# Kernel tuning notes

Measured on AMD Instinct MI355X. Metric: run time of the kernel, lower is better.

Reference implementation:

```python
import jax, jax.numpy as jnp
import numpy as np
import math

N = 50000        # nodes
E = 800000       # edges
FEATS = 64
CLASSES = 16
HIDDEN = 64
DEPTH = 10
DIFF = 0.9
EMB_DIM = 1 + int(math.log2(FEATS))   # 7
ADJ_HID = 4 + EMB_DIM                  # 11


def setup_inputs() -> dict:
    key = jax.random.key(0)
    ks = jax.random.split(key, 12)
    x = jax.random.normal(ks[0], (N, FEATS), dtype=jnp.float32)
    src = jax.random.randint(ks[1], (E,), 0, N, dtype=jnp.int64)
    dst = jax.random.randint(ks[2], (E,), 0, N, dtype=jnp.int64)
    s = 0.05
    W1 = jax.random.normal(ks[3], (2 * FEATS, HIDDEN), jnp.float32) * s
    b1 = jnp.zeros((HIDDEN,), jnp.float32)
    W2 = jax.random.normal(ks[4], (HIDDEN, CLASSES), jnp.float32) * s
    b2 = jnp.zeros((CLASSES,), jnp.float32)
    A1 = jax.random.normal(ks[5], (2 + EMB_DIM, ADJ_HID), jnp.float32) * s
    ab1 = jnp.zeros((ADJ_HID,), jnp.float32)
    A2 = jax.random.normal(ks[6], (ADJ_HID, 1), jnp.float32) * s
    ab2 = jnp.zeros((1,), jnp.float32)
    emb = jax.random.normal(ks[7], (FEATS, EMB_DIM), jnp.float32) * s
    return {"x": x, "src": src, "dst": dst, "W1": W1, "b1": b1,
            "W2": W2, "b2": b2, "A1": A1, "ab1": ab1, "A2": A2,
            "ab2": ab2, "emb": emb}


def reference(x, src, dst, W1, b1, W2, b2, A1, ab1, A2, ab2, emb):
    n, f = x.shape
    # cached symmetric GCN normalization: D^-1/2 A D^-1/2
    deg = jax.ops.segment_sum(jnp.ones((src.shape[0],), x.dtype), dst, num_segments=n)
    inv_sqrt = jnp.where(deg > 0, jax.lax.rsqrt(jnp.maximum(deg, 1e-12)), 0.0)
    norm = inv_sqrt[src] * inv_sqrt[dst]   # [E]

    def conv(z):
        return jax.ops.segment_sum(z[src] * norm[:, None], dst, num_segments=n)

    # first diffusion loop (personalized-pagerank style residual blend)
    h0 = x
    z = x
    for _ in range(DEPTH):
        z = conv(z) * DIFF + (1.0 - DIFF) * h0

    # node x class pair MLP (class-major flatten, matching x.t().reshape(-1,1))
    cls = jnp.repeat(jnp.arange(f), n)                 # [f*n]
    pairs = jnp.concatenate([z.T.reshape(-1, 1),
                             h0.T.reshape(-1, 1),
                             emb[cls]], axis=1)        # [f*n, 2+EMB_DIM]
    u = jax.nn.relu(pairs @ A1 + ab1)
    u = (u @ A2 + ab2) / 2.0                           # [f*n, 1]
    z = u.reshape(f, n).T                              # [n, f]

    # dropout is identity in eval mode
    z = jnp.concatenate([z, h0], axis=1)               # [n, 2f]
    z = jax.nn.relu(z @ W1 + b1)
    z = z @ W2 + b2                                    # [n, classes]

    # second diffusion loop over class logits
    g0 = z
    for _ in range(DEPTH):
        z = conv(z) * DIFF + (1.0 - DIFF) * g0
    return z
```

## Files before the change

kernel.cpp:

```cpp
#include <hip/hip_runtime.h>

#define FEATS    64
#define CLASSES  16
#define EMB_DIM  7
#define ADJ_HID  11
#define DIFF     0.9f

__device__ inline float bf2f(unsigned short u) {
    return __uint_as_float(((unsigned int)u) << 16);
}
__device__ inline unsigned short f2bf(float f) {
    unsigned int u = __float_as_uint(f);
    return (unsigned short)((u + 0x7FFFu + ((u >> 16) & 1u)) >> 16);
}


__global__ __launch_bounds__(256) void k_deg(const int* __restrict__ dst, int* __restrict__ deg, int e) {
    int i = blockIdx.x * 256 + threadIdx.x;
    if (i < e) atomicAdd(&deg[dst[i]], 1);
}

__global__ __launch_bounds__(256) void k_invs(const int* __restrict__ deg, float* __restrict__ invs, int n) {
    int i = blockIdx.x * 256 + threadIdx.x;
    if (i < n) { int d = deg[i]; invs[i] = d > 0 ? rsqrtf((float)d) : 0.f; }
}

__global__ __launch_bounds__(256) void k_scan1(const int* __restrict__ deg, int* __restrict__ rowptr,
                                               int* __restrict__ bsum, int n) {
    __shared__ int s[256];
    int tid = threadIdx.x;
    int i = blockIdx.x * 256 + tid;
    int v = (i < n) ? deg[i] : 0;
    s[tid] = v; __syncthreads();
    for (int ofs = 1; ofs < 256; ofs <<= 1) {
        int t = (tid >= ofs) ? s[tid - ofs] : 0;
        __syncthreads(); s[tid] += t; __syncthreads();
    }
    if (i < n) rowptr[i] = s[tid] - v;
    if (tid == 255) bsum[blockIdx.x] = s[255];
}

__global__ __launch_bounds__(256) void k_scan2(int* __restrict__ bsum, int nb) {
    __shared__ int s[256];
    int tid = threadIdx.x;
    int v = (tid < nb) ? bsum[tid] : 0;
    s[tid] = v; __syncthreads();
    for (int ofs = 1; ofs < 256; ofs <<= 1) {
        int t = (tid >= ofs) ? s[tid - ofs] : 0;
        __syncthreads(); s[tid] += t; __syncthreads();
    }
    if (tid < nb) bsum[tid] = s[tid] - v;
}

__global__ __launch_bounds__(256) void k_scan3(int* __restrict__ rowptr, const int* __restrict__ bsum,
                                               int n, int e) {
    int i = blockIdx.x * 256 + threadIdx.x;
    if (i < n) rowptr[i] += bsum[i >> 8];
    if (i == n) rowptr[n] = e;
}

__global__ __launch_bounds__(256) void k_scatter(const int* __restrict__ src, const int* __restrict__ dst,
                                                 const float* __restrict__ invs, const int* __restrict__ rowptr,
                                                 int* __restrict__ cnt, int2* __restrict__ edge, int e) {
    int i = blockIdx.x * 256 + threadIdx.x;
    if (i >= e) return;
    int d = dst[i], sv = src[i];
    int pos = rowptr[d] + atomicAdd(&cnt[d], 1);
    edge[pos] = make_int2(sv, __float_as_int(invs[sv] * invs[d]));
}


__global__ __launch_bounds__(256) void k_cast(const float4* __restrict__ in, ushort4* __restrict__ out, int total4) {
    int i = blockIdx.x * 256 + threadIdx.x;
    if (i < total4) {
        float4 v = in[i];
        ushort4 o;
        o.x = f2bf(v.x); o.y = f2bf(v.y); o.z = f2bf(v.z); o.w = f2bf(v.w);
        out[i] = o;
    }
}


__global__ __launch_bounds__(256) void k_conv64b(const ushort4* __restrict__ zin, const float4* __restrict__ h04,
                                                 ushort4* __restrict__ zout, const int* __restrict__ rowptr,
                                                 const int2* __restrict__ edge, int n) {
    int wid = (blockIdx.x * 256 + threadIdx.x) >> 6;
    if (wid >= n) return;
    int lane = threadIdx.x & 63;
    int g = lane >> 4, c = lane & 15;
    int e0 = rowptr[wid], e1 = rowptr[wid + 1];
    float a0 = 0.f, a1 = 0.f, a2 = 0.f, a3 = 0.f;
    for (int e = e0; e < e1; e += 16) {
        #pragma unroll
        for (int k = 0; k < 4; ++k) {
            int idx = e + k * 4 + g;
            bool ok = idx < e1;
            int2 p = edge[ok ? idx : e0];
            float w = ok ? __int_as_float(p.y) : 0.f;
            ushort4 v = zin[(size_t)p.x * 16 + c];
            a0 = fmaf(w, bf2f(v.x), a0);
            a1 = fmaf(w, bf2f(v.y), a1);
            a2 = fmaf(w, bf2f(v.z), a2);
            a3 = fmaf(w, bf2f(v.w), a3);
        }
    }
    a0 += __shfl_xor(a0, 16); a1 += __shfl_xor(a1, 16);
    a2 += __shfl_xor(a2, 16); a3 += __shfl_xor(a3, 16);
    a0 += __shfl_xor(a0, 32); a1 += __shfl_xor(a1, 32);
    a2 += __shfl_xor(a2, 32); a3 += __shfl_xor(a3, 32);
    if (lane < 16) {
        float4 h = h04[(size_t)wid * 16 + lane];
        ushort4 o;
        o.x = f2bf(a0 * DIFF + (1.f - DIFF) * h.x);
        o.y = f2bf(a1 * DIFF + (1.f - DIFF) * h.y);
        o.z = f2bf(a2 * DIFF + (1.f - DIFF) * h.z);
        o.w = f2bf(a3 * DIFF + (1.f - DIFF) * h.w);
        zout[(size_t)wid * 16 + lane] = o;
    }
}


__global__ __launch_bounds__(256) void k_conv16(const float4* __restrict__ zin4, const float4* __restrict__ g04,
                                                float4* __restrict__ zout4, const int* __restrict__ rowptr,
                                                const int2* __restrict__ edge, int n) {
    int wid = (blockIdx.x * 256 + threadIdx.x) >> 6;
    if (wid >= n) return;
    int lane = threadIdx.x & 63;
    int g = lane >> 2, c = lane & 3;
    int e0 = rowptr[wid], e1 = rowptr[wid + 1];
    float4 acc; acc.x = acc.y = acc.z = acc.w = 0.f;
    for (int e = e0; e < e1; e += 32) {
        #pragma unroll
        for (int k = 0; k < 2; ++k) {
            int idx = e + k * 16 + g;
            bool ok = idx < e1;
            int2 p = edge[ok ? idx : e0];
            float w = ok ? __int_as_float(p.y) : 0.f;
            float4 v = zin4[(size_t)p.x * 4 + c];
            acc.x = fmaf(w, v.x, acc.x);
            acc.y = fmaf(w, v.y, acc.y);
            acc.z = fmaf(w, v.z, acc.z);
            acc.w = fmaf(w, v.w, acc.w);
        }
    }
    float4 t;
    t.x = __shfl_xor(acc.x, 4);  t.y = __shfl_xor(acc.y, 4);  t.z = __shfl_xor(acc.z, 4);  t.w = __shfl_xor(acc.w, 4);
    acc.x += t.x; acc.y += t.y; acc.z += t.z; acc.w += t.w;
    t.x = __shfl_xor(acc.x, 8);  t.y = __shfl_xor(acc.y, 8);  t.z = __shfl_xor(acc.z, 8);  t.w = __shfl_xor(acc.w, 8);
    acc.x += t.x; acc.y += t.y; acc.z += t.z; acc.w += t.w;
    t.x = __shfl_xor(acc.x, 16); t.y = __shfl_xor(acc.y, 16); t.z = __shfl_xor(acc.z, 16); t.w = __shfl_xor(acc.w, 16);
    acc.x += t.x; acc.y += t.y; acc.z += t.z; acc.w += t.w;
    t.x = __shfl_xor(acc.x, 32); t.y = __shfl_xor(acc.y, 32); t.z = __shfl_xor(acc.z, 32); t.w = __shfl_xor(acc.w, 32);
    acc.x += t.x; acc.y += t.y; acc.z += t.z; acc.w += t.w;
    if (lane < 4) {
        float4 h = g04[(size_t)wid * 4 + lane];
        float4 o;
        o.x = acc.x * DIFF + (1.f - DIFF) * h.x;
        o.y = acc.y * DIFF + (1.f - DIFF) * h.y;
        o.z = acc.z * DIFF + (1.f - DIFF) * h.z;
        o.w = acc.w * DIFF + (1.f - DIFF) * h.w;
        zout4[(size_t)wid * 4 + lane] = o;
    }
}


__global__ __launch_bounds__(256) void k_pairmlp(const unsigned short* __restrict__ z1, const float* __restrict__ x,
                                                 const float* __restrict__ W1, const float* __restrict__ b1,
                                                 const float* __restrict__ W2, const float* __restrict__ b2,
                                                 const float* __restrict__ A1, const float* __restrict__ ab1,
                                                 const float* __restrict__ A2, const float* __restrict__ ab2,
                                                 const float* __restrict__ emb,
                                                 float* __restrict__ g0, int n) {
    __shared__ float W2s[64 * 16];
    __shared__ float in_s[32][128];
    __shared__ float hid[32 * 65];
    __shared__ float eA1[64 * ADJ_HID];
    __shared__ float a0s[ADJ_HID], a1s[ADJ_HID], a2s[ADJ_HID];
    __shared__ float ab2s;

    int tid  = threadIdx.x;
    int base = blockIdx.x * 32;

    #pragma unroll
    for (int k = 0; k < 4; ++k)  W2s[tid + k * 256] = W2[tid + k * 256];
    if (tid < ADJ_HID) { a0s[tid] = A1[tid]; a1s[tid] = A1[ADJ_HID + tid]; a2s[tid] = A2[tid]; }
    if (tid == 0) ab2s = ab2[0];
    for (int idx = tid; idx < 64 * ADJ_HID; idx += 256) {
        int c = idx / ADJ_HID, h = idx - c * ADJ_HID;
        float s = ab1[h];
        #pragma unroll
        for (int j = 0; j < EMB_DIM; j++) s = fmaf(emb[c * EMB_DIM + j], A1[(2 + j) * ADJ_HID + h], s);
        eA1[idx] = s;
    }
    __syncthreads();

    #pragma unroll
    for (int k = 0; k < 8; ++k) {
        int idx = tid + k * 256;
        int nl = idx >> 6, c = idx & 63;
        int node = base + nl; if (node > n - 1) node = n - 1;
        float zv = bf2f(z1[(size_t)node * 64 + c]);
        float xv = x[(size_t)node * 64 + c];
        float out = ab2s;
        #pragma unroll
        for (int h = 0; h < ADJ_HID; h++) {
            float t = fmaf(zv, a0s[h], fmaf(xv, a1s[h], eA1[c * ADJ_HID + h]));
            t = fmaxf(t, 0.f);
            out = fmaf(t, a2s[h], out);
        }
        in_s[nl][c]      = out * 0.5f;
        in_s[nl][64 + c] = xv;
    }
    __syncthreads();

    {
        int lane = tid & 63, wv = tid >> 6;
        int nb0 = wv * 8;
        float bv = b1[lane];
        float acc[8];
        #pragma unroll
        for (int j = 0; j < 8; ++j) acc[j] = bv;
        #pragma unroll 8
        for (int rb = 0; rb < 128; rb += 4) {
            float w0 = W1[(rb    ) * 64 + lane];
            float w1 = W1[(rb + 1) * 64 + lane];
            float w2 = W1[(rb + 2) * 64 + lane];
            float w3 = W1[(rb + 3) * 64 + lane];
            #pragma unroll
            for (int j = 0; j < 8; ++j) {
                float4 iv = *(const float4*)&in_s[nb0 + j][rb];
                acc[j] = fmaf(iv.w, w3, fmaf(iv.z, w2, fmaf(iv.y, w1, fmaf(iv.x, w0, acc[j]))));
            }
        }
        #pragma unroll
        for (int j = 0; j < 8; ++j) hid[(nb0 + j) * 65 + lane] = fmaxf(acc[j], 0.f);
    }
    __syncthreads();

    {
        int c  = tid & 15;
        int nl = tid >> 4;
        float ac0 = b2[c], ac1 = ac0;
        #pragma unroll
        for (int h = 0; h < 64; ++h) {
            float w = W2s[h * 16 + c];
            ac0 = fmaf(hid[nl * 65 + h],        w, ac0);
            ac1 = fmaf(hid[(nl + 16) * 65 + h], w, ac1);
        }
        int n0 = base + nl, n1 = base + nl + 16;
        if (n0 < n) g0[(size_t)n0 * 16 + c] = ac0;
        if (n1 < n) g0[(size_t)n1 * 16 + c] = ac1;
    }
}


extern "C" void kernel_launch(void* const* d_in, const int* in_sizes, int n_in,
                              void* d_out, int out_size, void* d_ws, size_t ws_size,
                              hipStream_t stream) {
    const float* x   = (const float*)d_in[0];
    const int*   src = (const int*)d_in[1];
    const int*   dst = (const int*)d_in[2];
    const float* W1  = (const float*)d_in[3];
    const float* b1  = (const float*)d_in[4];
    const float* W2  = (const float*)d_in[5];
    const float* b2  = (const float*)d_in[6];
    const float* A1  = (const float*)d_in[7];
    const float* ab1 = (const float*)d_in[8];
    const float* A2  = (const float*)d_in[9];
    const float* ab2 = (const float*)d_in[10];
    const float* emb = (const float*)d_in[11];

    int n = in_sizes[0] / FEATS;
    int e = in_sizes[1];

    char* ws = (char*)d_ws;
    size_t off = 0;
    auto alloc = [&](size_t bytes) {
        void* p = ws + off;
        off += bytes;
        off = (off + 255) & ~(size_t)255;
        return p;
    };

    int*     deg    = (int*)    alloc((size_t)n * 4);
    float*   invs   = (float*)  alloc((size_t)n * 4);
    int*     rowptr = (int*)    alloc((size_t)(n + 1) * 4);
    int*     cnt    = (int*)    alloc((size_t)n * 4);
    int*     bsum   = (int*)    alloc(1024);
    int2*    edge   = (int2*)   alloc((size_t)e * 8 + 256);
    ushort4* zbA    = (ushort4*)alloc((size_t)n * 64 * 2);
    ushort4* zbB    = (ushort4*)alloc((size_t)n * 64 * 2);
    float*   g0     = (float*)  alloc((size_t)n * 16 * 4);
    float*   g1     = (float*)  alloc((size_t)n * 16 * 4);
    float*   g2     = (float*)  alloc((size_t)n * 16 * 4);

    hipMemsetAsync(deg, 0, (size_t)n * 4, stream);
    hipMemsetAsync(cnt, 0, (size_t)n * 4, stream);

    int eb = (e + 255) / 256;
    int nb = (n + 255) / 256;

    k_deg    <<<eb, 256, 0, stream>>>(dst, deg, e);
    k_invs   <<<nb, 256, 0, stream>>>(deg, invs, n);
    k_scan1  <<<nb, 256, 0, stream>>>(deg, rowptr, bsum, n);
    k_scan2  <<<1, 256, 0, stream>>>(bsum, nb);
    k_scan3  <<<(n + 256) / 256, 256, 0, stream>>>(rowptr, bsum, n, e);
    k_scatter<<<eb, 256, 0, stream>>>(src, dst, invs, rowptr, cnt, edge, e);

    int total4 = n * 16;
    k_cast<<<(total4 + 255) / 256, 256, 0, stream>>>((const float4*)x, zbA, total4);

    int nwb = (n + 3) / 4;

    const ushort4* zin = zbA;
    ushort4* zout = zbB;
    for (int it = 0; it < 10; ++it) {
        k_conv64b<<<nwb, 256, 0, stream>>>(zin, (const float4*)x, zout, rowptr, edge, n);
        zin  = zout;
        zout = (zout == zbA) ? zbB : zbA;
    }
    const unsigned short* z1 = (const unsigned short*)zin;

    k_pairmlp<<<(n + 31) / 32, 256, 0, stream>>>(z1, x, W1, b1, W2, b2,
                                                 A1, ab1, A2, ab2, emb, g0, n);

    const float* gin = g0;
    float* gout = g1;
    for (int it = 0; it < 10; ++it) {
        float* out = (it == 9) ? (float*)d_out : gout;
        k_conv16<<<nwb, 256, 0, stream>>>((const float4*)gin, (const float4*)g0, (float4*)out,
                                          rowptr, edge, n);
        gin  = out;
        gout = (gout == g1) ? g2 : g1;
    }
}
```

Measured before the change: 706.1 us.

## Use bf16 residual in diffusion and persistent pair-MLP with shared-memory W1

The first diffusion loop now reads its residual h0 from a bf16 copy of x instead of fp32, which halves that read traffic in every iteration. The pair-MLP kernel becomes persistent with a fixed grid of 512 blocks looping over tiles. It stages W1 in shared memory once per block and vectorises the pair computation with ushort4/float4 loads and a transposed eA1 table. The bf16 residual adds rounding error to h0, and the kernel now uses about 50KB of shared memory, which can limit occupancy.

```diff
diff --git a/kernel.cpp b/kernel.cpp
--- a/kernel.cpp
+++ b/kernel.cpp
@@ -81,7 +81,7 @@
 }
 
 
-__global__ __launch_bounds__(256) void k_conv64b(const ushort4* __restrict__ zin, const float4* __restrict__ h04,
+__global__ __launch_bounds__(256) void k_conv64b(const ushort4* __restrict__ zin, const ushort4* __restrict__ h0b,
                                                  ushort4* __restrict__ zout, const int* __restrict__ rowptr,
                                                  const int2* __restrict__ edge, int n) {
     int wid = (blockIdx.x * 256 + threadIdx.x) >> 6;
@@ -109,12 +109,12 @@
     a0 += __shfl_xor(a0, 32); a1 += __shfl_xor(a1, 32);
     a2 += __shfl_xor(a2, 32); a3 += __shfl_xor(a3, 32);
     if (lane < 16) {
-        float4 h = h04[(size_t)wid * 16 + lane];
+        ushort4 h4 = h0b[(size_t)wid * 16 + lane];
         ushort4 o;
-        o.x = f2bf(a0 * DIFF + (1.f - DIFF) * h.x);
-        o.y = f2bf(a1 * DIFF + (1.f - DIFF) * h.y);
-        o.z = f2bf(a2 * DIFF + (1.f - DIFF) * h.z);
-        o.w = f2bf(a3 * DIFF + (1.f - DIFF) * h.w);
+        o.x = f2bf(a0 * DIFF + (1.f - DIFF) * bf2f(h4.x));
+        o.y = f2bf(a1 * DIFF + (1.f - DIFF) * bf2f(h4.y));
+        o.z = f2bf(a2 * DIFF + (1.f - DIFF) * bf2f(h4.z));
+        o.w = f2bf(a3 * DIFF + (1.f - DIFF) * bf2f(h4.w));
         zout[(size_t)wid * 16 + lane] = o;
     }
 }
@@ -164,92 +164,108 @@
 }
 
 
+#define PM_GRID 512
+
 __global__ __launch_bounds__(256) void k_pairmlp(const unsigned short* __restrict__ z1, const float* __restrict__ x,
                                                  const float* __restrict__ W1, const float* __restrict__ b1,
                                                  const float* __restrict__ W2, const float* __restrict__ b2,
                                                  const float* __restrict__ A1, const float* __restrict__ ab1,
                                                  const float* __restrict__ A2, const float* __restrict__ ab2,
                                                  const float* __restrict__ emb,
-                                                 float* __restrict__ g0, int n) {
+                                                 float* __restrict__ g0, int n, int ntiles) {
+    __shared__ float W1s[128 * 64];
     __shared__ float W2s[64 * 16];
     __shared__ float in_s[32][128];
     __shared__ float hid[32 * 65];
-    __shared__ float eA1[64 * ADJ_HID];
+    __shared__ float eA1T[ADJ_HID * 64];
     __shared__ float a0s[ADJ_HID], a1s[ADJ_HID], a2s[ADJ_HID];
     __shared__ float ab2s;
 
-    int tid  = threadIdx.x;
-    int base = blockIdx.x * 32;
-
+    int tid = threadIdx.x;
+    const ushort4* z4p = (const ushort4*)z1;
+    const float4*  x4p = (const float4*)x;
+
+    #pragma unroll
+    for (int k = 0; k < 32; ++k) W1s[tid + k * 256] = W1[tid + k * 256];
     #pragma unroll
     for (int k = 0; k < 4; ++k)  W2s[tid + k * 256] = W2[tid + k * 256];
     if (tid < ADJ_HID) { a0s[tid] = A1[tid]; a1s[tid] = A1[ADJ_HID + tid]; a2s[tid] = A2[tid]; }
     if (tid == 0) ab2s = ab2[0];
-    for (int idx = tid; idx < 64 * ADJ_HID; idx += 256) {
-        int c = idx / ADJ_HID, h = idx - c * ADJ_HID;
+    for (int idx = tid; idx < ADJ_HID * 64; idx += 256) {
+        int h = idx >> 6, c = idx & 63;
         float s = ab1[h];
         #pragma unroll
         for (int j = 0; j < EMB_DIM; j++) s = fmaf(emb[c * EMB_DIM + j], A1[(2 + j) * ADJ_HID + h], s);
-        eA1[idx] = s;
+        eA1T[idx] = s;
     }
     __syncthreads();
 
-    #pragma unroll
-    for (int k = 0; k < 8; ++k) {
-        int idx = tid + k * 256;
-        int nl = idx >> 6, c = idx & 63;
-        int node = base + nl; if (node > n - 1) node = n - 1;
-        float zv = bf2f(z1[(size_t)node * 64 + c]);
-        float xv = x[(size_t)node * 64 + c];
-        float out = ab2s;
+    for (int tile = blockIdx.x; tile < ntiles; tile += PM_GRID) {
+        int base = tile * 32;
+
         #pragma unroll
-        for (int h = 0; h < ADJ_HID; h++) {
-            float t = fmaf(zv, a0s[h], fmaf(xv, a1s[h], eA1[c * ADJ_HID + h]));
-            t = fmaxf(t, 0.f);
-            out = fmaf(t, a2s[h], out);
-        }
-        in_s[nl][c]      = out * 0.5f;
-        in_s[nl][64 + c] = xv;
-    }
-    __syncthreads();
-
-    {
-        int lane = tid & 63, wv = tid >> 6;
-        int nb0 = wv * 8;
-        float bv = b1[lane];
-        float acc[8];
-        #pragma unroll
-        for (int j = 0; j < 8; ++j) acc[j] = bv;
-        #pragma unroll 8
-        for (int rb = 0; rb < 128; rb += 4) {
-            float w0 = W1[(rb    ) * 64 + lane];
-            float w1 = W1[(rb + 1) * 64 + lane];
-            float w2 = W1[(rb + 2) * 64 + lane];
-            float w3 = W1[(rb + 3) * 64 + lane];
+        for (int j = 0; j < 2; ++j) {
+            int e4 = tid + j * 256;
+            int nl = e4 >> 4, c4 = e4 & 15;
+            int node = base + nl; if (node > n - 1) node = n - 1;
+            ushort4 z4 = z4p[(size_t)node * 16 + c4];
+            float4  x4 = x4p[(size_t)node * 16 + c4];
+            float zf0 = bf2f(z4.x), zf1 = bf2f(z4.y), zf2 = bf2f(z4.z), zf3 = bf2f(z4.w);
+            float o0 = ab2s, o1 = ab2s, o2 = ab2s, o3 = ab2s;
             #pragma unroll
-            for (int j = 0; j < 8; ++j) {
-                float4 iv = *(const float4*)&in_s[nb0 + j][rb];
-                acc[j] = fmaf(iv.w, w3, fmaf(iv.z, w2, fmaf(iv.y, w1, fmaf(iv.x, w0, acc[j]))));
+            for (int h = 0; h < ADJ_HID; h++) {
+                float a0 = a0s[h], a1 = a1s[h], a2 = a2s[h];
+                float4 ee = *(const float4*)&eA1T[h * 64 + c4 * 4];
+                float t;
+                t = fmaf(zf0, a0, fmaf(x4.x, a1, ee.x)); t = fmaxf(t, 0.f); o0 = fmaf(t, a2, o0);
+                t = fmaf(zf1, a0, fmaf(x4.y, a1, ee.y)); t = fmaxf(t, 0.f); o1 = fmaf(t, a2, o1);
+                t = fmaf(zf2, a0, fmaf(x4.z, a1, ee.z)); t = fmaxf(t, 0.f); o2 = fmaf(t, a2, o2);
+                t = fmaf(zf3, a0, fmaf(x4.w, a1, ee.w)); t = fmaxf(t, 0.f); o3 = fmaf(t, a2, o3);
             }
-        }
-        #pragma unroll
-        for (int j = 0; j < 8; ++j) hid[(nb0 + j) * 65 + lane] = fmaxf(acc[j], 0.f);
-    }
-    __syncthreads();
-
-    {
-        int c  = tid & 15;
-        int nl = tid >> 4;
-        float ac0 = b2[c], ac1 = ac0;
-        #pragma unroll
-        for (int h = 0; h < 64; ++h) {
-            float w = W2s[h * 16 + c];
-            ac0 = fmaf(hid[nl * 65 + h],        w, ac0);
-            ac1 = fmaf(hid[(nl + 16) * 65 + h], w, ac1);
-        }
-        int n0 = base + nl, n1 = base + nl + 16;
-        if (n0 < n) g0[(size_t)n0 * 16 + c] = ac0;
-        if (n1 < n) g0[(size_t)n1 * 16 + c] = ac1;
+            *(float4*)&in_s[nl][c4 * 4]      = make_float4(o0 * 0.5f, o1 * 0.5f, o2 * 0.5f, o3 * 0.5f);
+            *(float4*)&in_s[nl][64 + c4 * 4] = x4;
+        }
+        __syncthreads();
+
+        {
+            int lane = tid & 63, wv = tid >> 6;
+            int nb0 = wv * 8;
+            float bv = b1[lane];
+            float acc[8];
+            #pragma unroll
+            for (int j = 0; j < 8; ++j) acc[j] = bv;
+            #pragma unroll 8
+            for (int rb = 0; rb < 128; rb += 4) {
+                float w0 = W1s[(rb    ) * 64 + lane];
+                float w1 = W1s[(rb + 1) * 64 + lane];
+                float w2 = W1s[(rb + 2) * 64 + lane];
+                float w3 = W1s[(rb + 3) * 64 + lane];
+                #pragma unroll
+                for (int j = 0; j < 8; ++j) {
+                    float4 iv = *(const float4*)&in_s[nb0 + j][rb];
+                    acc[j] = fmaf(iv.w, w3, fmaf(iv.z, w2, fmaf(iv.y, w1, fmaf(iv.x, w0, acc[j]))));
+                }
+            }
+            #pragma unroll
+            for (int j = 0; j < 8; ++j) hid[(nb0 + j) * 65 + lane] = fmaxf(acc[j], 0.f);
+        }
+        __syncthreads();
+
+        {
+            int c  = tid & 15;
+            int nl = tid >> 4;
+            float ac0 = b2[c], ac1 = ac0;
+            #pragma unroll
+            for (int h = 0; h < 64; ++h) {
+                float w = W2s[h * 16 + c];
+                ac0 = fmaf(hid[nl * 65 + h],        w, ac0);
+                ac1 = fmaf(hid[(nl + 16) * 65 + h], w, ac1);
+            }
+            int n0 = base + nl, n1 = base + nl + 16;
+            if (n0 < n) g0[(size_t)n0 * 16 + c] = ac0;
+            if (n1 < n) g0[(size_t)n1 * 16 + c] = ac1;
+        }
+        __syncthreads();
     }
 }
 
@@ -288,6 +304,7 @@
     int*     cnt    = (int*)    alloc((size_t)n * 4);
     int*     bsum   = (int*)    alloc(1024);
     int2*    edge   = (int2*)   alloc((size_t)e * 8 + 256);
+    ushort4* xb     = (ushort4*)alloc((size_t)n * 64 * 2);
     ushort4* zbA    = (ushort4*)alloc((size_t)n * 64 * 2);
     ushort4* zbB    = (ushort4*)alloc((size_t)n * 64 * 2);
     float*   g0     = (float*)  alloc((size_t)n * 16 * 4);
@@ -308,21 +325,22 @@
     k_scatter<<<eb, 256, 0, stream>>>(src, dst, invs, rowptr, cnt, edge, e);
 
     int total4 = n * 16;
-    k_cast<<<(total4 + 255) / 256, 256, 0, stream>>>((const float4*)x, zbA, total4);
+    k_cast<<<(total4 + 255) / 256, 256, 0, stream>>>((const float4*)x, xb, total4);
 
     int nwb = (n + 3) / 4;
 
-    const ushort4* zin = zbA;
-    ushort4* zout = zbB;
+    const ushort4* zin = xb;
+    ushort4* zout = zbA;
     for (int it = 0; it < 10; ++it) {
-        k_conv64b<<<nwb, 256, 0, stream>>>(zin, (const float4*)x, zout, rowptr, edge, n);
+        k_conv64b<<<nwb, 256, 0, stream>>>(zin, xb, zout, rowptr, edge, n);
         zin  = zout;
-        zout = (zout == zbA) ? zbB : zbA;
+        zout = (it == 0) ? zbB : ((zout == zbA) ? zbB : zbA);
     }
     const unsigned short* z1 = (const unsigned short*)zin;
 
-    k_pairmlp<<<(n + 31) / 32, 256, 0, stream>>>(z1, x, W1, b1, W2, b2,
-                                                 A1, ab1, A2, ab2, emb, g0, n);
+    int ntiles = (n + 31) / 32;
+    k_pairmlp<<<PM_GRID, 256, 0, stream>>>(z1, x, W1, b1, W2, b2,
+                                           A1, ab1, A2, ab2, emb, g0, n, ntiles);
 
     const float* gin = g0;
     float* gout = g1;
```

Measured after the change: 683.3 us. 3.2% less time.
